# Performance work log

Measured on AMD Instinct MI355X. Metric: run time of the kernel, lower is better.

Reference implementation:

```python
import jax, jax.numpy as jnp
import numpy as np

N, D_IN, D_OUT = 2048, 128, 64


def setup_inputs() -> dict:
    key = jax.random.key(0)
    k1, k2, k3, k4 = jax.random.split(key, 4)
    node_features = jax.random.normal(k1, (N, D_IN), dtype=jnp.float32)
    neighbor_mask = jax.random.randint(k2, (N, N), 0, 2) > 0
    W = jax.random.normal(k3, (D_OUT, D_IN), dtype=jnp.float32) * (1.0 / np.sqrt(D_IN))
    a = jax.random.normal(k4, (2 * D_OUT,), dtype=jnp.float32)
    return {"node_features": node_features, "neighbor_mask": neighbor_mask, "W": W, "a": a}


def reference(node_features, neighbor_mask, W, a):
    # h = Linear(node_features): [N, D_OUT]
    h = node_features @ W.T
    d = h.shape[-1]
    # Additive-attention decomposition: einsum('ijn,n->ij', cat[h_i,h_j], a)
    # == (h @ a[:d])_i + (h @ a[d:])_j  -- same math, no NxNx2D tensor.
    s_i = h @ a[:d]  # [N]
    s_j = h @ a[d:]  # [N]
    scores = jax.nn.leaky_relu(s_i[:, None] + s_j[None, :], negative_slope=0.01)  # [N, N]
    neg_inf = jnp.array(-jnp.inf, dtype=scores.dtype)
    scores = jnp.where(neighbor_mask, scores, neg_inf)
    valid = jnp.any(neighbor_mask, axis=1, keepdims=True)  # [N, 1]
    scores = jnp.where(valid, scores, 0.0)
    alpha = jax.nn.softmax(scores, axis=1)
    alpha = jnp.where(neighbor_mask, alpha, 0.0)
    # messages[i, j, :] = alpha[i, j] * h[j]
    messages = alpha[:, :, None] * h[None, :, :]  # [N, N, D_OUT]
    return messages
```

## Files before the change

### kernel.cpp

```cpp
#include <hip/hip_runtime.h>
#include <math.h>

#define GN 2048
#define GD_IN 128
#define GD_OUT 64

typedef float f4 __attribute__((ext_vector_type(4)));
typedef int   i4 __attribute__((ext_vector_type(4)));

__global__ __launch_bounds__(64) void gat_h_kernel(
    const float* __restrict__ x,
    const float* __restrict__ W,
    const float* __restrict__ a,
    float* __restrict__ h,
    float* __restrict__ s_i,
    float* __restrict__ s_j) {
    __shared__ float wl[GD_OUT * (GD_IN + 1)];
    __shared__ float xl[GD_IN];
    const int i = blockIdx.x;
    const int t = threadIdx.x;

    for (int idx = t; idx < GD_OUT * GD_IN; idx += 64) {
        int o = idx >> 7, k = idx & 127;
        wl[o * (GD_IN + 1) + k] = W[idx];
    }
    xl[t]      = x[i * GD_IN + t];
    xl[t + 64] = x[i * GD_IN + t + 64];
    __syncthreads();

    float acc = 0.f;
    const float* wr = &wl[t * (GD_IN + 1)];
    #pragma unroll
    for (int k = 0; k < GD_IN; ++k) acc = fmaf(xl[k], wr[k], acc);
    h[i * GD_OUT + t] = acc;

    float p1 = acc * a[t];
    float p2 = acc * a[GD_OUT + t];
    #pragma unroll
    for (int off = 32; off; off >>= 1) {
        p1 += __shfl_down(p1, off);
        p2 += __shfl_down(p2, off);
    }
    if (t == 0) { s_i[i] = p1; s_j[i] = p2; }
}

__global__ __launch_bounds__(256) void gat_msg_kernel(
    const int* __restrict__ mask,
    const float* __restrict__ h,
    const float* __restrict__ s_i,
    const float* __restrict__ s_j,
    float* __restrict__ out) {
    __shared__ f4 sc4[GN / 4];
    __shared__ float red[4];
    const int i = blockIdx.x;
    const int t = threadIdx.x;
    const float si = s_i[i];

    const i4* __restrict__ mask4 = reinterpret_cast<const i4*>(mask) + (size_t)i * (GN / 4);
    const f4* __restrict__ sj4 = reinterpret_cast<const f4*>(s_j);
    float* sc = reinterpret_cast<float*>(sc4);

    float lmax = -INFINITY;
    #pragma unroll
    for (int q = t; q < GN / 4; q += 256) {
        i4 m = mask4[q];
        f4 sj = sj4[q];
        f4 s;
        #pragma unroll
        for (int k = 0; k < 4; ++k) {
            float z = si + sj[k];
            float v = z > 0.f ? z : 0.01f * z;
            s[k] = m[k] ? v : -INFINITY;
            lmax = fmaxf(lmax, s[k]);
        }
        sc4[q] = s;
    }
    #pragma unroll
    for (int off = 32; off; off >>= 1) lmax = fmaxf(lmax, __shfl_down(lmax, off));
    if ((t & 63) == 0) red[t >> 6] = lmax;
    __syncthreads();
    float rmax = fmaxf(fmaxf(red[0], red[1]), fmaxf(red[2], red[3]));
    if (rmax == -INFINITY) rmax = 0.f;

    float lsum = 0.f;
    #pragma unroll
    for (int q = t; q < GN / 4; q += 256) {
        f4 s = sc4[q];
        #pragma unroll
        for (int k = 0; k < 4; ++k) {
            s[k] = __expf(s[k] - rmax);
            lsum += s[k];
        }
        sc4[q] = s;
    }
    #pragma unroll
    for (int off = 32; off; off >>= 1) lsum += __shfl_down(lsum, off);
    __syncthreads();
    if ((t & 63) == 0) red[t >> 6] = lsum;
    __syncthreads();
    const float ssum = red[0] + red[1] + red[2] + red[3];
    const float inv = ssum > 0.f ? 1.f / ssum : 0.f;

    #pragma unroll
    for (int q = t; q < GN / 4; q += 256) sc4[q] *= inv;
    __syncthreads();

    const f4* __restrict__ h4 = reinterpret_cast<const f4*>(h);
    f4* __restrict__ out4 = reinterpret_cast<f4*>(out) + (size_t)i * GN * (GD_OUT / 4);
    const int jl = t >> 4;
    const int o4 = t & 15;
    const int rot = (i << 4) & (GN - 1);
    #pragma unroll 4
    for (int jb = 0; jb < GN; jb += 16) {
        int j = ((jb + rot) & (GN - 1)) + jl;
        float al = sc[j];
        f4 hv = h4[j * (GD_OUT / 4) + o4];
        out4[(size_t)j * (GD_OUT / 4) + o4] = hv * al;
    }
}

extern "C" void kernel_launch(void* const* d_in, const int* in_sizes, int n_in,
                              void* d_out, int out_size, void* d_ws, size_t ws_size,
                              hipStream_t stream) {
    const float* x    = (const float*)d_in[0];
    const int*   mask = (const int*)d_in[1];
    const float* W    = (const float*)d_in[2];
    const float* a    = (const float*)d_in[3];
    float* out = (float*)d_out;

    float* ws  = (float*)d_ws;
    float* h   = ws;
    float* s_i = ws + GN * GD_OUT;
    float* s_j = s_i + GN;

    gat_h_kernel<<<GN, 64, 0, stream>>>(x, W, a, h, s_i, s_j);
    gat_msg_kernel<<<GN, 256, 0, stream>>>(mask, h, s_i, s_j, out);
}
```

Measured before the change: 245.5 us.

## Process four rows per block with wave-level softmax and shared h loads

Each 256-thread block now handles four output rows, one wavefront per row. The softmax is computed entirely in registers with xor-shuffle reductions, so the block-level shared-memory reductions and most barriers go away. In the store phase each h vector is loaded once and reused for four rows, which cuts h reads fourfold. The row-dependent rotation of the j order is removed, and the grid shrinks to 512 blocks, which may lower occupancy or change how the 1 GB output write is distributed across memory channels.

```diff
diff --git a/kernel.cpp b/kernel.cpp
--- a/kernel.cpp
+++ b/kernel.cpp
@@ -50,72 +50,67 @@
     const float* __restrict__ s_i,
     const float* __restrict__ s_j,
     float* __restrict__ out) {
-    __shared__ f4 sc4[GN / 4];
-    __shared__ float red[4];
-    const int i = blockIdx.x;
+    __shared__ f4 alph4[4][GN / 4];
     const int t = threadIdx.x;
-    const float si = s_i[i];
+    const int w = t >> 6;
+    const int lane = t & 63;
+    const int i0 = blockIdx.x << 2;
+    const int row = i0 + w;
 
-    const i4* __restrict__ mask4 = reinterpret_cast<const i4*>(mask) + (size_t)i * (GN / 4);
+    const float si = s_i[row];
+    const i4* __restrict__ mask4 = reinterpret_cast<const i4*>(mask) + (size_t)row * (GN / 4);
     const f4* __restrict__ sj4 = reinterpret_cast<const f4*>(s_j);
-    float* sc = reinterpret_cast<float*>(sc4);
 
+    f4 s[8];
     float lmax = -INFINITY;
     #pragma unroll
-    for (int q = t; q < GN / 4; q += 256) {
+    for (int k = 0; k < 8; ++k) {
+        int q = k * 64 + lane;
         i4 m = mask4[q];
         f4 sj = sj4[q];
-        f4 s;
         #pragma unroll
-        for (int k = 0; k < 4; ++k) {
-            float z = si + sj[k];
+        for (int c = 0; c < 4; ++c) {
+            float z = si + sj[c];
             float v = z > 0.f ? z : 0.01f * z;
-            s[k] = m[k] ? v : -INFINITY;
-            lmax = fmaxf(lmax, s[k]);
+            s[k][c] = m[c] ? v : -INFINITY;
+            lmax = fmaxf(lmax, s[k][c]);
         }
-        sc4[q] = s;
     }
     #pragma unroll
-    for (int off = 32; off; off >>= 1) lmax = fmaxf(lmax, __shfl_down(lmax, off));
-    if ((t & 63) == 0) red[t >> 6] = lmax;
-    __syncthreads();
-    float rmax = fmaxf(fmaxf(red[0], red[1]), fmaxf(red[2], red[3]));
-    if (rmax == -INFINITY) rmax = 0.f;
+    for (int off = 32; off; off >>= 1) lmax = fmaxf(lmax, __shfl_xor(lmax, off));
+    float rmax = lmax == -INFINITY ? 0.f : lmax;
 
     float lsum = 0.f;
     #pragma unroll
-    for (int q = t; q < GN / 4; q += 256) {
-        f4 s = sc4[q];
+    for (int k = 0; k < 8; ++k) {
         #pragma unroll
-        for (int k = 0; k < 4; ++k) {
-            s[k] = __expf(s[k] - rmax);
-            lsum += s[k];
+        for (int c = 0; c < 4; ++c) {
+            s[k][c] = __expf(s[k][c] - rmax);
+            lsum += s[k][c];
         }
-        sc4[q] = s;
     }
     #pragma unroll
-    for (int off = 32; off; off >>= 1) lsum += __shfl_down(lsum, off);
-    __syncthreads();
-    if ((t & 63) == 0) red[t >> 6] = lsum;
-    __syncthreads();
-    const float ssum = red[0] + red[1] + red[2] + red[3];
-    const float inv = ssum > 0.f ? 1.f / ssum : 0.f;
+    for (int off = 32; off; off >>= 1) lsum += __shfl_xor(lsum, off);
+    const float inv = lsum > 0.f ? 1.f / lsum : 0.f;
 
     #pragma unroll
-    for (int q = t; q < GN / 4; q += 256) sc4[q] *= inv;
+    for (int k = 0; k < 8; ++k) alph4[w][k * 64 + lane] = s[k] * inv;
     __syncthreads();
 
+    const float* alpha = reinterpret_cast<const float*>(alph4);
     const f4* __restrict__ h4 = reinterpret_cast<const f4*>(h);
-    f4* __restrict__ out4 = reinterpret_cast<f4*>(out) + (size_t)i * GN * (GD_OUT / 4);
+    f4* __restrict__ out4 = reinterpret_cast<f4*>(out);
     const int jl = t >> 4;
     const int o4 = t & 15;
-    const int rot = (i << 4) & (GN - 1);
-    #pragma unroll 4
+    #pragma unroll 2
     for (int jb = 0; jb < GN; jb += 16) {
-        int j = ((jb + rot) & (GN - 1)) + jl;
-        float al = sc[j];
-        f4 hv = h4[j * (GD_OUT / 4) + o4];
-        out4[(size_t)j * (GD_OUT / 4) + o4] = hv * al;
+        const int j = jb + jl;
+        const f4 hv = h4[j * (GD_OUT / 4) + o4];
+        #pragma unroll
+        for (int ii = 0; ii < 4; ++ii) {
+            float al = alpha[ii * GN + j];
+            out4[((size_t)(i0 + ii) * GN + j) * (GD_OUT / 4) + o4] = hv * al;
+        }
     }
 }
 
@@ -134,5 +129,5 @@
     float* s_j = s_i + GN;
 
     gat_h_kernel<<<GN, 64, 0, stream>>>(x, W, a, h, s_i, s_j);
-    gat_msg_kernel<<<GN, 256, 0, stream>>>(mask, h, s_i, s_j, out);
+    gat_msg_kernel<<<GN / 4, 256, 0, stream>>>(mask, h, s_i, s_j, out);
 }
```

After: 217.5 us (median of 2 runs). 1.13x faster.
